# Kernel optimization log

Measured on AMD Instinct MI355X. Metric: run time of the kernel, lower is better.

## Reference

```python
import jax, jax.numpy as jnp
from jax import lax
import numpy as np

DN = ('NCHW', 'OIHW', 'NCHW')


def bilinear_grid_sample(x, grid):
    """F.grid_sample(x, grid) with mode='bilinear', padding_mode='zeros', align_corners=False.
    x: [N,C,H,W], grid: [N,Hg,Wg,2] with grid[...,0]=x(width) coord, grid[...,1]=y(height)."""
    N, C, H, W = x.shape
    gx, gy = grid[..., 0], grid[..., 1]
    ix = ((gx + 1.0) * W - 1.0) * 0.5  # unnormalize (align_corners=False)
    iy = ((gy + 1.0) * H - 1.0) * 0.5
    x0 = jnp.floor(ix); y0 = jnp.floor(iy)
    x1 = x0 + 1.0;      y1 = y0 + 1.0
    x_nhwc = jnp.transpose(x, (0, 2, 3, 1))  # [N,H,W,C]
    b = jnp.arange(N)[:, None, None]

    def gather(xi, yi):
        valid = (xi >= 0) & (xi <= W - 1) & (yi >= 0) & (yi <= H - 1)
        xc = jnp.clip(xi, 0, W - 1).astype(jnp.int32)
        yc = jnp.clip(yi, 0, H - 1).astype(jnp.int32)
        return x_nhwc[b, yc, xc] * valid[..., None].astype(x.dtype)  # [N,Hg,Wg,C]

    wa = ((x1 - ix) * (y1 - iy))[..., None]
    wb = ((x1 - ix) * (iy - y0))[..., None]
    wc = ((ix - x0) * (y1 - iy))[..., None]
    wd = ((ix - x0) * (iy - y0))[..., None]
    out = (gather(x0, y0) * wa + gather(x0, y1) * wb
           + gather(x1, y0) * wc + gather(x1, y1) * wd)
    return jnp.transpose(out, (0, 3, 1, 2))  # [N,C,Hg,Wg]


def setup_inputs() -> dict:
    key = jax.random.key(0)
    k1, k2, k3, k4 = jax.random.split(key, 4)
    N, C, H, W, Cout = 8, 64, 256, 256, 64
    x = jax.random.normal(k1, (N, C, H, W), dtype=jnp.float32)
    # original zero-inits conv_deform; use tiny random weights so offsets are small but non-trivial
    w_def = jax.random.normal(k2, (2, C, 5, 5), dtype=jnp.float32) * 0.01
    b_def = jnp.zeros((2,), dtype=jnp.float32)
    w_conv = jax.random.normal(k3, (Cout, C, 3, 3), dtype=jnp.float32) * (1.0 / np.sqrt(C * 9))
    b_conv = jax.random.normal(k4, (Cout,), dtype=jnp.float32) * 0.01
    return {"x": x, "w_def": w_def, "b_def": b_def, "w_conv": w_conv, "b_conv": b_conv}


def reference(x, w_def, b_def, w_conv, b_conv):
    N, C, H, W = x.shape
    # offset branch: conv2d(in->2, k=5, pad=2), to NHWC
    off = lax.conv_general_dilated(x, w_def, (1, 1), [(2, 2), (2, 2)], dimension_numbers=DN)
    off = jnp.transpose(off, (0, 2, 3, 1)) + b_def  # [N,H,W,2]
    # regular grid: meshgrid(ij) of linspace over H then W, cat[xx,yy]
    xx, yy = jnp.meshgrid(jnp.linspace(-1.0, 1.0, H), jnp.linspace(-1.0, 1.0, W), indexing='ij')
    grid = off + jnp.stack([xx, yy], axis=-1)[None].astype(x.dtype)
    xs = bilinear_grid_sample(x, grid)
    out = lax.conv_general_dilated(xs, w_conv, (1, 1), [(1, 1), (1, 1)], dimension_numbers=DN)
    return out + b_conv[None, :, None, None]
```

## Files before the change

kernel.cpp:

```cpp
#include <hip/hip_runtime.h>

typedef unsigned int u32;
typedef __attribute__((ext_vector_type(8))) short short8;
typedef __attribute__((ext_vector_type(4))) float f32x4;

__device__ __forceinline__ unsigned short f2bf(float f){
  u32 u = __builtin_bit_cast(u32, f);
  u = u + 0x7fffu + ((u >> 16) & 1u);
  return (unsigned short)(u >> 16);
}
__device__ __forceinline__ float bf2f(unsigned short h){
  return __builtin_bit_cast(float, ((u32)h) << 16);
}

__global__ __launch_bounds__(256) void k_pack_b(const float* __restrict__ w_conv,
                                                unsigned short* __restrict__ Bp){
  int idx = blockIdx.x*256 + threadIdx.x;
  if (idx >= 9*2*4*64*8) return;
  int i    = idx & 7;
  int lane = (idx >> 3) & 63;
  int t    = (idx >> 9) & 3;
  int chunk= (idx >> 11) & 1;
  int tap  = idx >> 12;
  int co = t*16 + (lane & 15);
  int c  = chunk*32 + (lane >> 4)*8 + i;
  int ki = tap/3, kj = tap%3;
  Bp[idx] = f2bf(w_conv[((co*64 + c)*3 + ki)*3 + kj]);
}

__global__ __launch_bounds__(256) void k_transpose(const float* __restrict__ x,
                                                   unsigned short* __restrict__ xn){
  __shared__ float tile[64][65];
  int n = blockIdx.y, pix0 = blockIdx.x*64;
  int tid = threadIdx.x, lane = tid & 63, grp = tid >> 6;
  #pragma unroll
  for (int k = 0; k < 16; k++){
    int c = k*4 + grp;
    tile[c][lane] = x[(n*64 + c)*65536 + pix0 + lane];
  }
  __syncthreads();
  #pragma unroll
  for (int k = 0; k < 16; k++){
    int p = k*4 + grp;
    xn[(n*65536 + pix0 + p)*64 + lane] = f2bf(tile[lane][p]);
  }
}

__global__ __launch_bounds__(256) void k_offset(const float* __restrict__ x,
                                                const float* __restrict__ w_def,
                                                const float* __restrict__ b_def,
                                                float2* __restrict__ gridc){
  __shared__ float red[4][4][2][256];
  int b = blockIdx.x;
  int xcd  = b & 7;
  int w8   = b >> 3;
  int qloc = w8 & 7;
  int n    = w8 >> 3;
  int i0   = (xcd*8 + qloc)*4;
  int tid = threadIdx.x, l = tid & 63;
  int wv = __builtin_amdgcn_readfirstlane(tid >> 6);

  float me0 = (l == 0)  ? 0.f : 1.f;
  float me1 = (l == 63) ? 0.f : 1.f;
  int o0 = (l == 0)  ? 0 : -2;
  int o3 = (l == 63) ? 2 : 4;

  float a0[4][4], a1[4][4];
  #pragma unroll
  for (int s = 0; s < 4; s++)
    #pragma unroll
    for (int q = 0; q < 4; q++){ a0[s][q] = 0.f; a1[s][q] = 0.f; }

  for (int cc = 0; cc < 16; cc++){
    int c = (wv << 4) + cc;
    const float* rp  = x + ((n << 6) + c)*65536 + (l << 2);
    const float* wq0 = w_def + c*25;
    const float* wq1 = w_def + 1600 + c*25;
    float w0[25], w1[25];
    #pragma unroll
    for (int t = 0; t < 25; t++){ w0[t] = wq0[t]; w1[t] = wq1[t]; }

    #pragma unroll
    for (int r = 0; r < 8; r++){
      int gi = i0 - 2 + r;
      if (gi < 0 || gi > 255) continue;
      const float* rr = rp + (gi << 8);
      float2 d0 = *(const float2*)(rr + o0);
      float2 d1 = *(const float2*)(rr);
      float2 d2 = *(const float2*)(rr + 2);
      float2 d3 = *(const float2*)(rr + o3);
      float wd[8];
      wd[0] = d0.x * me0; wd[1] = d0.y * me0;
      wd[2] = d1.x;       wd[3] = d1.y;
      wd[4] = d2.x;       wd[5] = d2.y;
      wd[6] = d3.x * me1; wd[7] = d3.y * me1;
      #pragma unroll
      for (int s = 0; s < 4; s++){
        int ki = r - s;
        if (ki < 0 || ki > 4) continue;
        #pragma unroll
        for (int q = 0; q < 4; q++)
          #pragma unroll
          for (int kj = 0; kj < 5; kj++){
            a0[s][q] = fmaf(wd[q+kj], w0[ki*5+kj], a0[s][q]);
            a1[s][q] = fmaf(wd[q+kj], w1[ki*5+kj], a1[s][q]);
          }
      }
    }
  }

  #pragma unroll
  for (int s = 0; s < 4; s++)
    #pragma unroll
    for (int q = 0; q < 4; q++){
      red[wv][s][0][(l << 2) + q] = a0[s][q];
      red[wv][s][1][(l << 2) + q] = a1[s][q];
    }
  __syncthreads();

  float bd0 = b_def[0], bd1 = b_def[1];
  #pragma unroll
  for (int v = 0; v < 4; v++){
    int p = tid + (v << 8);
    int s = p >> 8, col = p & 255;
    float s0 = red[0][s][0][col] + red[1][s][0][col] + red[2][s][0][col] + red[3][s][0][col];
    float s1 = red[0][s][1][col] + red[1][s][1][col] + red[2][s][1][col] + red[3][s][1][col];
    int i = i0 + s;
    float gx = s0 + bd0 + (-1.0f + (2.0f/255.0f)*(float)i);
    float gy = s1 + bd1 + (-1.0f + (2.0f/255.0f)*(float)col);
    float ix = ((gx + 1.0f)*256.0f - 1.0f)*0.5f;
    float iy = ((gy + 1.0f)*256.0f - 1.0f)*0.5f;
    gridc[((n << 8) + i)*256 + col] = make_float2(ix, iy);
  }
}

__global__ __launch_bounds__(256,2) void k_conv2s(const unsigned short* __restrict__ xn,
                                                  const float2* __restrict__ gridc,
                                                  const unsigned short* __restrict__ Bp,
                                                  const float* __restrict__ b_conv,
                                                  float* __restrict__ out){
  __shared__ unsigned char Al[324*128];
  int n = blockIdx.z, i0 = blockIdx.y*16, j0 = blockIdx.x*16;
  int tid = threadIdx.x, w = tid >> 6, l = tid & 63;

  int sub   = tid & 15;
  int pbase = tid >> 4;
  #pragma unroll 2
  for (int pass = 0; pass < 21; ++pass){
    int p = pass*16 + pbase;
    if (p < 324){
      int rr = p/18, cc = p - rr*18;
      int gi = i0 - 1 + rr, gj = j0 - 1 + cc;
      u32 pk0 = 0, pk1 = 0;
      if (gi >= 0 && gi < 256 && gj >= 0 && gj < 256){
        float2 g = gridc[(((n << 8) + gi) << 8) + gj];
        float ix = g.x, iy = g.y;
        float x0f = floorf(ix), y0f = floorf(iy);
        float fx = ix - x0f, fy = iy - y0f;
        int x0 = (int)x0f, y0 = (int)y0f;
        int x1 = x0 + 1, y1 = y0 + 1;
        float m00 = ((x0>=0)&(x0<256)&(y0>=0)&(y0<256)) ? 1.f : 0.f;
        float m01 = ((x0>=0)&(x0<256)&(y1>=0)&(y1<256)) ? 1.f : 0.f;
        float m10 = ((x1>=0)&(x1<256)&(y0>=0)&(y0<256)) ? 1.f : 0.f;
        float m11 = ((x1>=0)&(x1<256)&(y1>=0)&(y1<256)) ? 1.f : 0.f;
        int x0c = x0 < 0 ? 0 : (x0 > 255 ? 255 : x0);
        int x1c = x1 < 0 ? 0 : (x1 > 255 ? 255 : x1);
        int y0c = y0 < 0 ? 0 : (y0 > 255 ? 255 : y0);
        int y1c = y1 < 0 ? 0 : (y1 > 255 ? 255 : y1);
        int nb = n << 16, s4 = sub << 2;
        ushort4 v00 = *(const ushort4*)(xn + (((nb + (y0c<<8) + x0c) << 6) + s4));
        ushort4 v01 = *(const ushort4*)(xn + (((nb + (y1c<<8) + x0c) << 6) + s4));
        ushort4 v10 = *(const ushort4*)(xn + (((nb + (y0c<<8) + x1c) << 6) + s4));
        ushort4 v11 = *(const ushort4*)(xn + (((nb + (y1c<<8) + x1c) << 6) + s4));
        float w00 = (1.f-fx)*(1.f-fy)*m00;
        float w01 = (1.f-fx)*fy*m01;
        float w10 = fx*(1.f-fy)*m10;
        float w11 = fx*fy*m11;
        float r0 = bf2f(v00.x)*w00 + bf2f(v01.x)*w01 + bf2f(v10.x)*w10 + bf2f(v11.x)*w11;
        float r1 = bf2f(v00.y)*w00 + bf2f(v01.y)*w01 + bf2f(v10.y)*w10 + bf2f(v11.y)*w11;
        float r2 = bf2f(v00.z)*w00 + bf2f(v01.z)*w01 + bf2f(v10.z)*w10 + bf2f(v11.z)*w11;
        float r3 = bf2f(v00.w)*w00 + bf2f(v01.w)*w01 + bf2f(v10.w)*w10 + bf2f(v11.w)*w11;
        pk0 = (u32)f2bf(r0) | ((u32)f2bf(r1) << 16);
        pk1 = (u32)f2bf(r2) | ((u32)f2bf(r3) << 16);
      }
      int byte = ((p << 7) + (sub << 3)) ^ ((p & 7) << 4);
      *(uint2*)(Al + byte) = make_uint2(pk0, pk1);
    }
  }

  f32x4 zero = {0.f,0.f,0.f,0.f};
  f32x4 acc[4][4];
  #pragma unroll
  for (int m = 0; m < 4; m++)
    #pragma unroll
    for (int t = 0; t < 4; t++) acc[m][t] = zero;

  __syncthreads();

  const short8* bp8 = (const short8*)Bp;
  #pragma unroll
  for (int ki = 0; ki < 3; ki++)
    #pragma unroll
    for (int kj = 0; kj < 3; kj++)
      #pragma unroll
      for (int ch = 0; ch < 2; ch++){
        short8 bfr[4];
        #pragma unroll
        for (int t = 0; t < 4; t++)
          bfr[t] = bp8[(((ki*3 + kj)*2 + ch)*4 + t)*64 + l];
        short8 a[4];
        #pragma unroll
        for (int m = 0; m < 4; m++){
          int p = (w*4 + m + ki)*18 + (l & 15) + kj;
          int byte = (p*128 + ch*64 + ((l >> 4) << 4)) ^ ((p & 7) << 4);
          a[m] = *(const short8*)(Al + byte);
        }
        #pragma unroll
        for (int t = 0; t < 4; t++)
          #pragma unroll
          for (int m = 0; m < 4; m++)
            acc[m][t] = __builtin_amdgcn_mfma_f32_16x16x32_bf16(a[m], bfr[t], acc[m][t], 0, 0, 0);
      }

  int colp0 = (l >> 4) * 4;
  #pragma unroll
  for (int t = 0; t < 4; t++){
    int co = t*16 + (l & 15);
    float bias = b_conv[co];
    #pragma unroll
    for (int m = 0; m < 4; m++){
      int r = w*4 + m;
      f32x4 v = acc[m][t];
      v[0] += bias; v[1] += bias; v[2] += bias; v[3] += bias;
      *(f32x4*)(&out[(((n*64 + co)<<8) + i0 + r)*256 + j0 + colp0]) = v;
    }
  }
}

extern "C" void kernel_launch(void* const* d_in, const int* in_sizes, int n_in,
                              void* d_out, int out_size, void* d_ws, size_t ws_size,
                              hipStream_t stream) {
  const float* x      = (const float*)d_in[0];
  const float* w_def  = (const float*)d_in[1];
  const float* b_def  = (const float*)d_in[2];
  const float* w_conv = (const float*)d_in[3];
  const float* b_conv = (const float*)d_in[4];
  float* out = (float*)d_out;

  unsigned char* ws = (unsigned char*)d_ws;
  unsigned short* xn    = (unsigned short*)(ws);
  float2*         gridc = (float2*)(ws + 67108864);
  unsigned short* Bp    = (unsigned short*)(ws + 71303168);

  k_pack_b   <<<144, 256, 0, stream>>>(w_conv, Bp);
  k_transpose<<<dim3(1024, 8), 256, 0, stream>>>(x, xn);
  k_offset   <<<512, 256, 0, stream>>>(x, w_def, b_def, gridc);
  k_conv2s   <<<dim3(16, 16, 8), 256, 0, stream>>>(xn, gridc, Bp, b_conv, out);
}
```

Measured before the change: 415.6 us.

## Software-pipeline deformable gather staging and raise occupancy target to three blocks

The bilinear-gather staging loop becomes a two-deep software pipeline. Grid coordinates for later passes and the four corner loads for the next pass are issued before the previous pass's blend and LDS store, to hide global-memory latency. Out-of-range pass indices are clamped to the last patch position, which removes the branch at the cost of one redundant, harmless pass. The launch bound asks for three blocks per SIMD instead of two, which caps registers per thread and may cause spills given the 64-float accumulator.

```diff
diff --git a/kernel.cpp b/kernel.cpp
--- a/kernel.cpp
+++ b/kernel.cpp
@@ -134,7 +134,7 @@
   }
 }
 
-__global__ __launch_bounds__(256,2) void k_conv2s(const unsigned short* __restrict__ xn,
+__global__ __launch_bounds__(256,3) void k_conv2s(const unsigned short* __restrict__ xn,
                                                   const float2* __restrict__ gridc,
                                                   const unsigned short* __restrict__ Bp,
                                                   const float* __restrict__ b_conv,
@@ -142,51 +142,72 @@
   __shared__ unsigned char Al[324*128];
   int n = blockIdx.z, i0 = blockIdx.y*16, j0 = blockIdx.x*16;
   int tid = threadIdx.x, w = tid >> 6, l = tid & 63;
-
-  int sub   = tid & 15;
-  int pbase = tid >> 4;
-  #pragma unroll 2
-  for (int pass = 0; pass < 21; ++pass){
-    int p = pass*16 + pbase;
-    if (p < 324){
-      int rr = p/18, cc = p - rr*18;
-      int gi = i0 - 1 + rr, gj = j0 - 1 + cc;
-      u32 pk0 = 0, pk1 = 0;
-      if (gi >= 0 && gi < 256 && gj >= 0 && gj < 256){
-        float2 g = gridc[(((n << 8) + gi) << 8) + gj];
-        float ix = g.x, iy = g.y;
-        float x0f = floorf(ix), y0f = floorf(iy);
-        float fx = ix - x0f, fy = iy - y0f;
-        int x0 = (int)x0f, y0 = (int)y0f;
-        int x1 = x0 + 1, y1 = y0 + 1;
-        float m00 = ((x0>=0)&(x0<256)&(y0>=0)&(y0<256)) ? 1.f : 0.f;
-        float m01 = ((x0>=0)&(x0<256)&(y1>=0)&(y1<256)) ? 1.f : 0.f;
-        float m10 = ((x1>=0)&(x1<256)&(y0>=0)&(y0<256)) ? 1.f : 0.f;
-        float m11 = ((x1>=0)&(x1<256)&(y1>=0)&(y1<256)) ? 1.f : 0.f;
-        int x0c = x0 < 0 ? 0 : (x0 > 255 ? 255 : x0);
-        int x1c = x1 < 0 ? 0 : (x1 > 255 ? 255 : x1);
-        int y0c = y0 < 0 ? 0 : (y0 > 255 ? 255 : y0);
-        int y1c = y1 < 0 ? 0 : (y1 > 255 ? 255 : y1);
-        int nb = n << 16, s4 = sub << 2;
-        ushort4 v00 = *(const ushort4*)(xn + (((nb + (y0c<<8) + x0c) << 6) + s4));
-        ushort4 v01 = *(const ushort4*)(xn + (((nb + (y1c<<8) + x0c) << 6) + s4));
-        ushort4 v10 = *(const ushort4*)(xn + (((nb + (y0c<<8) + x1c) << 6) + s4));
-        ushort4 v11 = *(const ushort4*)(xn + (((nb + (y1c<<8) + x1c) << 6) + s4));
-        float w00 = (1.f-fx)*(1.f-fy)*m00;
-        float w01 = (1.f-fx)*fy*m01;
-        float w10 = fx*(1.f-fy)*m10;
-        float w11 = fx*fy*m11;
-        float r0 = bf2f(v00.x)*w00 + bf2f(v01.x)*w01 + bf2f(v10.x)*w10 + bf2f(v11.x)*w11;
-        float r1 = bf2f(v00.y)*w00 + bf2f(v01.y)*w01 + bf2f(v10.y)*w10 + bf2f(v11.y)*w11;
-        float r2 = bf2f(v00.z)*w00 + bf2f(v01.z)*w01 + bf2f(v10.z)*w10 + bf2f(v11.z)*w11;
-        float r3 = bf2f(v00.w)*w00 + bf2f(v01.w)*w01 + bf2f(v10.w)*w10 + bf2f(v11.w)*w11;
-        pk0 = (u32)f2bf(r0) | ((u32)f2bf(r1) << 16);
-        pk1 = (u32)f2bf(r2) | ((u32)f2bf(r3) << 16);
-      }
-      int byte = ((p << 7) + (sub << 3)) ^ ((p & 7) << 4);
-      *(uint2*)(Al + byte) = make_uint2(pk0, pk1);
-    }
-  }
+  int sub = tid & 15, pbase = tid >> 4;
+  const int nb = n << 16, s4 = sub << 2;
+
+#define STAGE_G(P, GQ) { \
+  int p_ = (P)*16 + pbase; if (p_ > 323) p_ = 323; \
+  int rr_ = p_/18, cc_ = p_ - rr_*18; \
+  int gi_ = i0 - 1 + rr_, gj_ = j0 - 1 + cc_; \
+  int gic_ = gi_ < 0 ? 0 : (gi_ > 255 ? 255 : gi_); \
+  int gjc_ = gj_ < 0 ? 0 : (gj_ > 255 ? 255 : gj_); \
+  GQ = gridc[nb + (gic_ << 8) + gjc_]; \
+}
+
+#define STAGE_S(P, GQ, WTS, BYTE, C00, C01, C10, C11) { \
+  int p_ = (P)*16 + pbase; if (p_ > 323) p_ = 323; \
+  int rr_ = p_/18, cc_ = p_ - rr_*18; \
+  int gi_ = i0 - 1 + rr_, gj_ = j0 - 1 + cc_; \
+  float ok_ = (gi_ >= 0 && gi_ < 256 && gj_ >= 0 && gj_ < 256) ? 1.f : 0.f; \
+  float ix_ = GQ.x, iy_ = GQ.y; \
+  float x0f_ = floorf(ix_), y0f_ = floorf(iy_); \
+  float fx_ = ix_ - x0f_, fy_ = iy_ - y0f_; \
+  int x0_ = (int)x0f_, y0_ = (int)y0f_; \
+  int x1_ = x0_ + 1, y1_ = y0_ + 1; \
+  float m00_ = (((x0_>=0)&(x0_<256)&(y0_>=0)&(y0_<256)) ? 1.f : 0.f) * ok_; \
+  float m01_ = (((x0_>=0)&(x0_<256)&(y1_>=0)&(y1_<256)) ? 1.f : 0.f) * ok_; \
+  float m10_ = (((x1_>=0)&(x1_<256)&(y0_>=0)&(y0_<256)) ? 1.f : 0.f) * ok_; \
+  float m11_ = (((x1_>=0)&(x1_<256)&(y1_>=0)&(y1_<256)) ? 1.f : 0.f) * ok_; \
+  int x0c_ = x0_ < 0 ? 0 : (x0_ > 255 ? 255 : x0_); \
+  int x1c_ = x1_ < 0 ? 0 : (x1_ > 255 ? 255 : x1_); \
+  int y0c_ = y0_ < 0 ? 0 : (y0_ > 255 ? 255 : y0_); \
+  int y1c_ = y1_ < 0 ? 0 : (y1_ > 255 ? 255 : y1_); \
+  C00 = *(const ushort4*)(xn + (((nb + (y0c_<<8) + x0c_) << 6) + s4)); \
+  C01 = *(const ushort4*)(xn + (((nb + (y1c_<<8) + x0c_) << 6) + s4)); \
+  C10 = *(const ushort4*)(xn + (((nb + (y0c_<<8) + x1c_) << 6) + s4)); \
+  C11 = *(const ushort4*)(xn + (((nb + (y1c_<<8) + x1c_) << 6) + s4)); \
+  WTS = make_float4((1.f-fx_)*(1.f-fy_)*m00_, (1.f-fx_)*fy_*m01_, \
+                    fx_*(1.f-fy_)*m10_,       fx_*fy_*m11_); \
+  BYTE = ((p_ << 7) + (sub << 3)) ^ ((p_ & 7) << 4); \
+}
+
+#define STAGE_L(WTS, BYTE, C00, C01, C10, C11) { \
+  float r0_ = bf2f(C00.x)*WTS.x + bf2f(C01.x)*WTS.y + bf2f(C10.x)*WTS.z + bf2f(C11.x)*WTS.w; \
+  float r1_ = bf2f(C00.y)*WTS.x + bf2f(C01.y)*WTS.y + bf2f(C10.y)*WTS.z + bf2f(C11.y)*WTS.w; \
+  float r2_ = bf2f(C00.z)*WTS.x + bf2f(C01.z)*WTS.y + bf2f(C10.z)*WTS.z + bf2f(C11.z)*WTS.w; \
+  float r3_ = bf2f(C00.w)*WTS.x + bf2f(C01.w)*WTS.y + bf2f(C10.w)*WTS.z + bf2f(C11.w)*WTS.w; \
+  u32 pk0_ = (u32)f2bf(r0_) | ((u32)f2bf(r1_) << 16); \
+  u32 pk1_ = (u32)f2bf(r2_) | ((u32)f2bf(r3_) << 16); \
+  *(uint2*)(Al + BYTE) = make_uint2(pk0_, pk1_); \
+}
+
+  float2 gA, gB; float4 wtsA, wtsB; int byteA, byteB;
+  ushort4 a00, a01, a10, a11, b00, b01, b10, b11;
+  STAGE_G(0, gA)
+  STAGE_G(1, gB)
+  STAGE_S(0, gA, wtsA, byteA, a00, a01, a10, a11)
+  #pragma unroll
+  for (int P = 0; P < 20; P += 2){
+    STAGE_S(P+1, gB, wtsB, byteB, b00, b01, b10, b11)
+    STAGE_G(P+2, gA)
+    STAGE_L(wtsA, byteA, a00, a01, a10, a11)
+    STAGE_S(P+2, gA, wtsA, byteA, a00, a01, a10, a11)
+    STAGE_G(P+3, gB)
+    STAGE_L(wtsB, byteB, b00, b01, b10, b11)
+  }
+  STAGE_S(21, gB, wtsB, byteB, b00, b01, b10, b11)
+  STAGE_L(wtsA, byteA, a00, a01, a10, a11)
+  STAGE_L(wtsB, byteB, b00, b01, b10, b11)
 
   f32x4 zero = {0.f,0.f,0.f,0.f};
   f32x4 acc[4][4];
```

Result: no change. 408.1 us (-1.8%).
